# Optimization experiments

Hardware: AMD Instinct MI355X
Metric: run time of the kernel (lower is better)

## Reference

```python
import jax, jax.numpy as jnp
import numpy as np

B, L, D = 4, 8192, 512


def setup_inputs() -> dict:
    key = jax.random.key(0)
    kx, kwg, kwc = jax.random.split(key, 3)
    x = jax.random.normal(kx, (B, L, D), dtype=jnp.float32)
    # Xavier-uniform init for DxD linears
    bound = float(np.sqrt(6.0 / (D + D)))
    Wg = jax.random.uniform(kwg, (D, D), minval=-bound, maxval=bound, dtype=jnp.float32)
    bg = jnp.ones((D,), dtype=jnp.float32)   # gate bias init to 1.0
    Wc = jax.random.uniform(kwc, (D, D), minval=-bound, maxval=bound, dtype=jnp.float32)
    bc = jnp.zeros((D,), dtype=jnp.float32)
    return {"x": x, "Wg": Wg, "bg": bg, "Wc": Wc, "bc": bc}


def _mingru_scan(gates, cands):
    # h_t = (1 - g_t) * h_{t-1} + g_t * c_t, h_0 = 0
    # linear recurrence h_t = a_t h_{t-1} + b_t with a = 1-g, b = g*c
    a = 1.0 - gates
    b = gates * cands

    def combine(left, right):
        a_l, b_l = left
        a_r, b_r = right
        return a_r * a_l, a_r * b_l + b_r

    _, h = jax.lax.associative_scan(combine, (a, b), axis=1)
    return h


def reference(x, Wg, bg, Wc, bc):
    gates = jax.nn.sigmoid(jnp.einsum('bld,ed->ble', x, Wg) + bg)
    cands = jnp.tanh(jnp.einsum('bld,ed->ble', x, Wc) + bc)
    return _mingru_scan(gates, cands)
```

## Files before the change

### kernel.cpp

```cpp
#include <hip/hip_runtime.h>
#include <stdint.h>
#include <stddef.h>

#define B_ 4
#define L_ 8192
#define D_ 512
#define M_ (B_*L_)
#define K_ 512
#define CHUNK 64
#define NC (L_/CHUNK)

typedef _Float16 f16;
typedef f16 f16x2 __attribute__((ext_vector_type(2)));
typedef f16 f16x4 __attribute__((ext_vector_type(4)));
typedef f16 f16x8 __attribute__((ext_vector_type(8)));
typedef float f32x4 __attribute__((ext_vector_type(4)));

__device__ __forceinline__ void async16(const void* g, void* l) {
  __builtin_amdgcn_global_load_lds(
      (const __attribute__((address_space(1))) uint32_t*)g,
      (__attribute__((address_space(3))) uint32_t*)l,
      16, 0, 0);
}

__global__ __launch_bounds__(256) void prep(const float* __restrict__ x,
                                            const float* __restrict__ Wg,
                                            const float* __restrict__ Wc,
                                            f16* __restrict__ xh,
                                            f16* __restrict__ wp) {
  const int bid = blockIdx.x;
  const int isX = (bid < 8192);
  const int U = (isX ? bid : (bid - 8192)) * 256 + threadIdx.x;
  const int r  = U >> 6;
  const int w_ = U & 63;
  const int s  = w_ >> 3;
  const int u3 = w_ & 7;
  const int du = (r << 6) + (s << 3) + (u3 ^ (r & 7));
  const float* src;
  if (isX)            src = x + (size_t)U * 8;
  else if (r < 512)   src = Wg + (size_t)r * 512 + w_ * 8;
  else                src = Wc + (size_t)(r - 512) * 512 + w_ * 8;
  float4 v0 = *(const float4*)src;
  float4 v1 = *(const float4*)(src + 4);
  f16x8 o = {(f16)v0.x, (f16)v0.y, (f16)v0.z, (f16)v0.w,
             (f16)v1.x, (f16)v1.y, (f16)v1.z, (f16)v1.w};
  f16* dst = isX ? xh : wp;
  *(f16x8*)(dst + (size_t)du * 8) = o;
}

__global__ __launch_bounds__(512, 2) void gemm_act(
    const f16* __restrict__ Xh, const f16* __restrict__ Wp,
    const float* __restrict__ bg, const float* __restrict__ bc,
    uint32_t* __restrict__ AC,
    float* __restrict__ cA, float* __restrict__ cB) {
  __shared__ __align__(16) f16 sA[2][256 * 64];
  __shared__ __align__(16) f16 sBg[2][128 * 64];
  __shared__ __align__(16) f16 sBc[2][128 * 64];

  const int tid = threadIdx.x;
  const int id = blockIdx.x;
  const int xcd = id & 7;
  const int slot = id >> 3;
  const int g_ = xcd * 64 + slot;
  const int bm = g_ >> 2;
  const int bn = g_ & 3;

  const int lane = tid & 63;
  const int w = tid >> 6;
  const int wm = w >> 1, wn = w & 1;
  const int l15 = lane & 15, quad = lane >> 4;

  const int srow = tid >> 3;
  const int sp8 = (tid & 7) * 8;
  const f16* gA  = Xh + (size_t)(bm * 256 + srow) * K_ + sp8;
  const f16* gBg = Wp + (size_t)(bn * 128 + srow) * K_ + sp8;
  const f16* gBc = Wp + (size_t)(512 + bn * 128 + srow) * K_ + sp8;

  const int xu0 = (quad ^ (l15 & 7)) * 8;
  const int xu1 = xu0 ^ 32;

  f32x4 accG[4][4] = {};
  f32x4 accC[4][4] = {};

#define STAGE(kk, b) { \
    async16(gA + (kk),                    &sA[b][tid * 8]); \
    async16(gA + (size_t) 64 * K_ + (kk), &sA[b][tid * 8 +  64 * 64]); \
    async16(gA + (size_t)128 * K_ + (kk), &sA[b][tid * 8 + 128 * 64]); \
    async16(gA + (size_t)192 * K_ + (kk), &sA[b][tid * 8 + 192 * 64]); \
    async16(gBg + (kk),                   &sBg[b][tid * 8]); \
    async16(gBg + (size_t)64 * K_ + (kk), &sBg[b][tid * 8 + 64 * 64]); \
    async16(gBc + (kk),                   &sBc[b][tid * 8]); \
    async16(gBc + (size_t)64 * K_ + (kk), &sBc[b][tid * 8 + 64 * 64]); }

#define COMPUTE(bC) { \
    _Pragma("unroll") \
    for (int k32 = 0; k32 < 2; k32++) { \
      const int xu = k32 ? xu1 : xu0; \
      f16x8 af[4], bgf[4], bcf[4]; \
      _Pragma("unroll") \
      for (int i = 0; i < 4; i++) \
        af[i] = *(const f16x8*)(&sA[bC][(wm * 64 + i * 16 + l15) * 64 + xu]); \
      _Pragma("unroll") \
      for (int j = 0; j < 4; j++) { \
        bgf[j] = *(const f16x8*)(&sBg[bC][(wn * 64 + j * 16 + l15) * 64 + xu]); \
        bcf[j] = *(const f16x8*)(&sBc[bC][(wn * 64 + j * 16 + l15) * 64 + xu]); \
      } \
      _Pragma("unroll") \
      for (int i = 0; i < 4; i++) \
        _Pragma("unroll") \
        for (int j = 0; j < 4; j++) { \
          accG[i][j] = __builtin_amdgcn_mfma_f32_16x16x32_f16(af[i], bgf[j], accG[i][j], 0, 0, 0); \
          accC[i][j] = __builtin_amdgcn_mfma_f32_16x16x32_f16(af[i], bcf[j], accC[i][j], 0, 0, 0); \
        } \
    } }

  STAGE(0, 0);
  asm volatile("s_waitcnt vmcnt(0)" ::: "memory");
  __builtin_amdgcn_s_barrier();

#pragma unroll
  for (int t = 0; t < 7; t++) {
    const int c = t & 1, n = c ^ 1;
    STAGE((t + 1) * 64, n);
    COMPUTE(c);
    asm volatile("s_waitcnt vmcnt(0)" ::: "memory");
    __builtin_amdgcn_s_barrier();
  }
  COMPUTE(1);
#undef COMPUTE
#undef STAGE

  const int c = bm * 4 + wm;
#pragma unroll
  for (int j = 0; j < 4; j++) {
    const int col = bn * 128 + wn * 64 + j * 16 + l15;
    const float bgv = bg[col];
    const float bcv = bc[col];
    float blkP[4], blkQ[4];
#pragma unroll
    for (int i = 0; i < 4; i++) {
      const int mrow = bm * 256 + wm * 64 + i * 16 + quad * 4;
      float P = 1.0f, Q = 0.0f;
#pragma unroll
      for (int r = 0; r < 4; r++) {
        float yg = accG[i][j][r] + bgv;
        float gg = 1.0f / (1.0f + __expf(-yg));
        float yc = accC[i][j][r] + bcv;
        yc = fminf(fmaxf(yc, -15.0f), 15.0f);
        float t = __expf(2.0f * yc);
        float cc = (t - 1.0f) / (t + 1.0f);
        f16x2 p;
        p[0] = (f16)(1.0f - gg);
        p[1] = (f16)(gg * cc);
        *(f16x2*)&AC[(size_t)(mrow + r) * 512 + col] = p;
        const float av = (float)p[0];
        const float bv = (float)p[1];
        Q = fmaf(av, Q, bv);
        P *= av;
      }
      float Pp = __shfl_xor(P, 16);
      float Qp = __shfl_xor(Q, 16);
      float nP = P * Pp;
      float nQ = (quad & 1) ? fmaf(P, Qp, Q) : fmaf(Pp, Q, Qp);
      Pp = __shfl_xor(nP, 32);
      Qp = __shfl_xor(nQ, 32);
      blkP[i] = nP * Pp;
      blkQ[i] = (quad & 2) ? fmaf(nP, Qp, nQ) : fmaf(Pp, nQ, Qp);
    }
    float CP = blkP[0], CQ = blkQ[0];
#pragma unroll
    for (int i = 1; i < 4; i++) {
      CQ = fmaf(blkP[i], CQ, blkQ[i]);
      CP *= blkP[i];
    }
    if (quad == 0) {
      cA[(size_t)c * 512 + col] = CP;
      cB[(size_t)c * 512 + col] = CQ;
    }
  }
}

__global__ __launch_bounds__(128) void scan_apply(
    const uint32_t* __restrict__ AC,
    const float* __restrict__ cA, const float* __restrict__ cB,
    float* __restrict__ out) {
  const int blk = blockIdx.x;
  const int ch = blk & (NC - 1);
  const int bseq = blk >> 7;
  const int d0 = threadIdx.x * 4;

  float h0 = 0.0f, h1 = 0.0f, h2 = 0.0f, h3 = 0.0f;
  const float* pA = cA + (size_t)(bseq * NC) * 512 + d0;
  const float* pB = cB + (size_t)(bseq * NC) * 512 + d0;
#pragma unroll 4
  for (int cc = 0; cc < ch; cc++) {
    float4 va = *(const float4*)(pA + (size_t)cc * 512);
    float4 vb = *(const float4*)(pB + (size_t)cc * 512);
    h0 = fmaf(va.x, h0, vb.x);
    h1 = fmaf(va.y, h1, vb.y);
    h2 = fmaf(va.z, h2, vb.z);
    h3 = fmaf(va.w, h3, vb.w);
  }

  const size_t base = (size_t)blk * CHUNK * 512 + d0;
#pragma unroll 8
  for (int t = 0; t < CHUNK; t++) {
    const size_t i = base + (size_t)t * 512;
    uint4 v = *(const uint4*)&AC[i];
    f16x2 p0 = __builtin_bit_cast(f16x2, v.x);
    f16x2 p1 = __builtin_bit_cast(f16x2, v.y);
    f16x2 p2 = __builtin_bit_cast(f16x2, v.z);
    f16x2 p3 = __builtin_bit_cast(f16x2, v.w);
    h0 = fmaf((float)p0[0], h0, (float)p0[1]);
    h1 = fmaf((float)p1[0], h1, (float)p1[1]);
    h2 = fmaf((float)p2[0], h2, (float)p2[1]);
    h3 = fmaf((float)p3[0], h3, (float)p3[1]);
    float4 o;
    o.x = h0; o.y = h1; o.z = h2; o.w = h3;
    *(float4*)&out[i] = o;
  }
}

extern "C" void kernel_launch(void* const* d_in, const int* in_sizes, int n_in,
                              void* d_out, int out_size, void* d_ws, size_t ws_size,
                              hipStream_t stream) {
  const float* x  = (const float*)d_in[0];
  const float* Wg = (const float*)d_in[1];
  const float* bg = (const float*)d_in[2];
  const float* Wc = (const float*)d_in[3];
  const float* bc = (const float*)d_in[4];
  float* out = (float*)d_out;

  char* ws = (char*)d_ws;
  f16*      xh = (f16*)(ws);
  f16*      wp = (f16*)(ws + 33554432);
  uint32_t* AC = (uint32_t*)(ws + 34603008);
  float*    cA = (float*)(ws + 101711872);
  float*    cB = (float*)(ws + 102760448);

  prep<<<8448, 256, 0, stream>>>(x, Wg, Wc, xh, wp);
  gemm_act<<<512, 512, 0, stream>>>(xh, wp, bg, bc, AC, cA, cB);
  scan_apply<<<B_ * NC, 128, 0, stream>>>(AC, cA, cB, out);
}
```

Baseline: 228.3 us.

## Fuse GEMM, chunk scan and apply into one persistent kernel with grid barriers

```diff
diff --git a/kernel.cpp b/kernel.cpp
--- a/kernel.cpp
+++ b/kernel.cpp
@@ -12,7 +12,6 @@
 
 typedef _Float16 f16;
 typedef f16 f16x2 __attribute__((ext_vector_type(2)));
-typedef f16 f16x4 __attribute__((ext_vector_type(4)));
 typedef f16 f16x8 __attribute__((ext_vector_type(8)));
 typedef float f32x4 __attribute__((ext_vector_type(4)));
 
@@ -21,6 +20,13 @@
       (const __attribute__((address_space(1))) uint32_t*)g,
       (__attribute__((address_space(3))) uint32_t*)l,
       16, 0, 0);
+}
+
+__device__ __forceinline__ float aload(const float* p) {
+  return __hip_atomic_load(p, __ATOMIC_RELAXED, __HIP_MEMORY_SCOPE_AGENT);
+}
+__device__ __forceinline__ void astore(float* p, float v) {
+  __hip_atomic_store(p, v, __ATOMIC_RELAXED, __HIP_MEMORY_SCOPE_AGENT);
 }
 
 __global__ __launch_bounds__(256) void prep(const float* __restrict__ x,
@@ -48,176 +54,206 @@
   *(f16x8*)(dst + (size_t)du * 8) = o;
 }
 
-__global__ __launch_bounds__(512, 2) void gemm_act(
+__device__ __forceinline__ void gbar(int* cnt, int target) {
+  __threadfence();
+  __syncthreads();
+  if (threadIdx.x == 0) {
+    atomicAdd(cnt, 1);
+    while (__hip_atomic_load(cnt, __ATOMIC_RELAXED, __HIP_MEMORY_SCOPE_AGENT) < target)
+      __builtin_amdgcn_s_sleep(8);
+  }
+  __syncthreads();
+  __threadfence();
+}
+
+__global__ __launch_bounds__(512, 2) void fused(
     const f16* __restrict__ Xh, const f16* __restrict__ Wp,
     const float* __restrict__ bg, const float* __restrict__ bc,
-    uint32_t* __restrict__ AC,
-    float* __restrict__ cA, float* __restrict__ cB) {
-  __shared__ __align__(16) f16 sA[2][256 * 64];
+    float* __restrict__ cA, float* __restrict__ cB,
+    float* __restrict__ Hpre, int* __restrict__ bar,
+    float* __restrict__ out) {
+  __shared__ __align__(16) f16 sA[2][128 * 64];
   __shared__ __align__(16) f16 sBg[2][128 * 64];
   __shared__ __align__(16) f16 sBc[2][128 * 64];
 
   const int tid = threadIdx.x;
   const int id = blockIdx.x;
-  const int xcd = id & 7;
-  const int slot = id >> 3;
-  const int g_ = xcd * 64 + slot;
-  const int bm = g_ >> 2;
-  const int bn = g_ & 3;
+  const int bm = (id & 7) * 32 + (id >> 3);
 
   const int lane = tid & 63;
   const int w = tid >> 6;
-  const int wm = w >> 1, wn = w & 1;
+  const int wm = w >> 2, wn = w & 3;
   const int l15 = lane & 15, quad = lane >> 4;
 
   const int srow = tid >> 3;
   const int sp8 = (tid & 7) * 8;
-  const f16* gA  = Xh + (size_t)(bm * 256 + srow) * K_ + sp8;
-  const f16* gBg = Wp + (size_t)(bn * 128 + srow) * K_ + sp8;
-  const f16* gBc = Wp + (size_t)(512 + bn * 128 + srow) * K_ + sp8;
+  const f16* gA  = Xh + (size_t)(bm * 128 + srow) * K_ + sp8;
+  const f16* gBg = Wp + (size_t)srow * K_ + sp8;
+  const f16* gBc = Wp + (size_t)(512 + srow) * K_ + sp8;
 
   const int xu0 = (quad ^ (l15 & 7)) * 8;
   const int xu1 = xu0 ^ 32;
 
-  f32x4 accG[4][4] = {};
-  f32x4 accC[4][4] = {};
-
-#define STAGE(kk, b) { \
-    async16(gA + (kk),                    &sA[b][tid * 8]); \
-    async16(gA + (size_t) 64 * K_ + (kk), &sA[b][tid * 8 +  64 * 64]); \
-    async16(gA + (size_t)128 * K_ + (kk), &sA[b][tid * 8 + 128 * 64]); \
-    async16(gA + (size_t)192 * K_ + (kk), &sA[b][tid * 8 + 192 * 64]); \
-    async16(gBg + (kk),                   &sBg[b][tid * 8]); \
-    async16(gBg + (size_t)64 * K_ + (kk), &sBg[b][tid * 8 + 64 * 64]); \
-    async16(gBc + (kk),                   &sBc[b][tid * 8]); \
-    async16(gBc + (size_t)64 * K_ + (kk), &sBc[b][tid * 8 + 64 * 64]); }
+  const int c_ = bm * 2 + wm;
+  uint4 ab[4][4][2];
+
+#define STAGE(kk, b, bo) { \
+    async16(gA + (kk),                   &sA[b][tid * 8]); \
+    async16(gA + (size_t)64 * K_ + (kk), &sA[b][tid * 8 + 64 * 64]); \
+    async16(gBg + (bo) + (kk),                   &sBg[b][tid * 8]); \
+    async16(gBg + (bo) + (size_t)64 * K_ + (kk), &sBg[b][tid * 8 + 64 * 64]); \
+    async16(gBc + (bo) + (kk),                   &sBc[b][tid * 8]); \
+    async16(gBc + (bo) + (size_t)64 * K_ + (kk), &sBc[b][tid * 8 + 64 * 64]); }
 
 #define COMPUTE(bC) { \
     _Pragma("unroll") \
     for (int k32 = 0; k32 < 2; k32++) { \
       const int xu = k32 ? xu1 : xu0; \
-      f16x8 af[4], bgf[4], bcf[4]; \
+      f16x8 af[4], bgf[2], bcf[2]; \
       _Pragma("unroll") \
       for (int i = 0; i < 4; i++) \
         af[i] = *(const f16x8*)(&sA[bC][(wm * 64 + i * 16 + l15) * 64 + xu]); \
       _Pragma("unroll") \
-      for (int j = 0; j < 4; j++) { \
-        bgf[j] = *(const f16x8*)(&sBg[bC][(wn * 64 + j * 16 + l15) * 64 + xu]); \
-        bcf[j] = *(const f16x8*)(&sBc[bC][(wn * 64 + j * 16 + l15) * 64 + xu]); \
+      for (int j = 0; j < 2; j++) { \
+        bgf[j] = *(const f16x8*)(&sBg[bC][(wn * 32 + j * 16 + l15) * 64 + xu]); \
+        bcf[j] = *(const f16x8*)(&sBc[bC][(wn * 32 + j * 16 + l15) * 64 + xu]); \
       } \
       _Pragma("unroll") \
       for (int i = 0; i < 4; i++) \
         _Pragma("unroll") \
-        for (int j = 0; j < 4; j++) { \
+        for (int j = 0; j < 2; j++) { \
           accG[i][j] = __builtin_amdgcn_mfma_f32_16x16x32_f16(af[i], bgf[j], accG[i][j], 0, 0, 0); \
           accC[i][j] = __builtin_amdgcn_mfma_f32_16x16x32_f16(af[i], bcf[j], accC[i][j], 0, 0, 0); \
         } \
     } }
 
-  STAGE(0, 0);
-  asm volatile("s_waitcnt vmcnt(0)" ::: "memory");
-  __builtin_amdgcn_s_barrier();
-
-#pragma unroll
-  for (int t = 0; t < 7; t++) {
-    const int c = t & 1, n = c ^ 1;
-    STAGE((t + 1) * 64, n);
-    COMPUTE(c);
+#pragma unroll
+  for (int bn = 0; bn < 4; bn++) {
+    const size_t bo = (size_t)bn * 128 * K_;
+    f32x4 accG[4][2] = {};
+    f32x4 accC[4][2] = {};
+
+    STAGE(0, 0, bo);
     asm volatile("s_waitcnt vmcnt(0)" ::: "memory");
     __builtin_amdgcn_s_barrier();
-  }
-  COMPUTE(1);
+#pragma unroll
+    for (int t = 0; t < 7; t++) {
+      const int cb = t & 1, nb = cb ^ 1;
+      STAGE((t + 1) * 64, nb, bo);
+      COMPUTE(cb);
+      asm volatile("s_waitcnt vmcnt(0)" ::: "memory");
+      __builtin_amdgcn_s_barrier();
+    }
+    COMPUTE(1);
+
+#pragma unroll
+    for (int j = 0; j < 2; j++) {
+      const int col = bn * 128 + wn * 32 + j * 16 + l15;
+      const float bgv = bg[col];
+      const float bcv = bc[col];
+      float blkP[4], blkQ[4];
+#pragma unroll
+      for (int i = 0; i < 4; i++) {
+        float P = 1.0f, Q = 0.0f;
+        uint32_t pk[4];
+#pragma unroll
+        for (int r = 0; r < 4; r++) {
+          float yg = accG[i][j][r] + bgv;
+          float gg = 1.0f / (1.0f + __expf(-yg));
+          float yc = accC[i][j][r] + bcv;
+          yc = fminf(fmaxf(yc, -15.0f), 15.0f);
+          float tt = __expf(2.0f * yc);
+          float cc = (tt - 1.0f) / (tt + 1.0f);
+          f16x2 p;
+          p[0] = (f16)(1.0f - gg);
+          p[1] = (f16)(gg * cc);
+          pk[r] = __builtin_bit_cast(uint32_t, p);
+          const float av = (float)p[0];
+          const float bv = (float)p[1];
+          Q = fmaf(av, Q, bv);
+          P *= av;
+        }
+        ab[bn][i][j] = make_uint4(pk[0], pk[1], pk[2], pk[3]);
+        float Pp = __shfl_xor(P, 16);
+        float Qp = __shfl_xor(Q, 16);
+        float nP = P * Pp;
+        float nQ = (quad & 1) ? fmaf(P, Qp, Q) : fmaf(Pp, Q, Qp);
+        Pp = __shfl_xor(nP, 32);
+        Qp = __shfl_xor(nQ, 32);
+        blkP[i] = nP * Pp;
+        blkQ[i] = (quad & 2) ? fmaf(nP, Qp, nQ) : fmaf(Pp, nQ, Qp);
+      }
+      float CP = blkP[0], CQ = blkQ[0];
+#pragma unroll
+      for (int i = 1; i < 4; i++) {
+        CQ = fmaf(blkP[i], CQ, blkQ[i]);
+        CP *= blkP[i];
+      }
+      if (quad == 0) {
+        astore(&cA[(size_t)c_ * 512 + col], CP);
+        astore(&cB[(size_t)c_ * 512 + col], CQ);
+      }
+    }
+  }
 #undef COMPUTE
 #undef STAGE
 
-  const int c = bm * 4 + wm;
-#pragma unroll
-  for (int j = 0; j < 4; j++) {
-    const int col = bn * 128 + wn * 64 + j * 16 + l15;
-    const float bgv = bg[col];
-    const float bcv = bc[col];
-    float blkP[4], blkQ[4];
-#pragma unroll
-    for (int i = 0; i < 4; i++) {
-      const int mrow = bm * 256 + wm * 64 + i * 16 + quad * 4;
-      float P = 1.0f, Q = 0.0f;
-#pragma unroll
-      for (int r = 0; r < 4; r++) {
-        float yg = accG[i][j][r] + bgv;
-        float gg = 1.0f / (1.0f + __expf(-yg));
-        float yc = accC[i][j][r] + bcv;
-        yc = fminf(fmaxf(yc, -15.0f), 15.0f);
-        float t = __expf(2.0f * yc);
-        float cc = (t - 1.0f) / (t + 1.0f);
-        f16x2 p;
-        p[0] = (f16)(1.0f - gg);
-        p[1] = (f16)(gg * cc);
-        *(f16x2*)&AC[(size_t)(mrow + r) * 512 + col] = p;
-        const float av = (float)p[0];
-        const float bv = (float)p[1];
-        Q = fmaf(av, Q, bv);
-        P *= av;
-      }
-      float Pp = __shfl_xor(P, 16);
-      float Qp = __shfl_xor(Q, 16);
-      float nP = P * Pp;
-      float nQ = (quad & 1) ? fmaf(P, Qp, Q) : fmaf(Pp, Q, Qp);
-      Pp = __shfl_xor(nP, 32);
-      Qp = __shfl_xor(nQ, 32);
-      blkP[i] = nP * Pp;
-      blkQ[i] = (quad & 2) ? fmaf(nP, Qp, nQ) : fmaf(Pp, nQ, Qp);
-    }
-    float CP = blkP[0], CQ = blkQ[0];
-#pragma unroll
-    for (int i = 1; i < 4; i++) {
-      CQ = fmaf(blkP[i], CQ, blkQ[i]);
-      CP *= blkP[i];
-    }
-    if (quad == 0) {
-      cA[(size_t)c * 512 + col] = CP;
-      cB[(size_t)c * 512 + col] = CQ;
-    }
-  }
-}
-
-__global__ __launch_bounds__(128) void scan_apply(
-    const uint32_t* __restrict__ AC,
-    const float* __restrict__ cA, const float* __restrict__ cB,
-    float* __restrict__ out) {
-  const int blk = blockIdx.x;
-  const int ch = blk & (NC - 1);
-  const int bseq = blk >> 7;
-  const int d0 = threadIdx.x * 4;
-
-  float h0 = 0.0f, h1 = 0.0f, h2 = 0.0f, h3 = 0.0f;
-  const float* pA = cA + (size_t)(bseq * NC) * 512 + d0;
-  const float* pB = cB + (size_t)(bseq * NC) * 512 + d0;
-#pragma unroll 4
-  for (int cc = 0; cc < ch; cc++) {
-    float4 va = *(const float4*)(pA + (size_t)cc * 512);
-    float4 vb = *(const float4*)(pB + (size_t)cc * 512);
-    h0 = fmaf(va.x, h0, vb.x);
-    h1 = fmaf(va.y, h1, vb.y);
-    h2 = fmaf(va.z, h2, vb.z);
-    h3 = fmaf(va.w, h3, vb.w);
-  }
-
-  const size_t base = (size_t)blk * CHUNK * 512 + d0;
-#pragma unroll 8
-  for (int t = 0; t < CHUNK; t++) {
-    const size_t i = base + (size_t)t * 512;
-    uint4 v = *(const uint4*)&AC[i];
-    f16x2 p0 = __builtin_bit_cast(f16x2, v.x);
-    f16x2 p1 = __builtin_bit_cast(f16x2, v.y);
-    f16x2 p2 = __builtin_bit_cast(f16x2, v.z);
-    f16x2 p3 = __builtin_bit_cast(f16x2, v.w);
-    h0 = fmaf((float)p0[0], h0, (float)p0[1]);
-    h1 = fmaf((float)p1[0], h1, (float)p1[1]);
-    h2 = fmaf((float)p2[0], h2, (float)p2[1]);
-    h3 = fmaf((float)p3[0], h3, (float)p3[1]);
-    float4 o;
-    o.x = h0; o.y = h1; o.z = h2; o.w = h3;
-    *(float4*)&out[i] = o;
+  gbar(bar, 256);
+
+  if (id < 4) {
+    const int seq = blockIdx.x & 3;
+    const int d = tid;
+    float h = 0.0f;
+    for (int ch = 0; ch < NC; ch++) {
+      const int idx = (seq * NC + ch) * 512 + d;
+      astore(&Hpre[idx], h);
+      h = fmaf(aload(&cA[idx]), h, aload(&cB[idx]));
+    }
+  }
+
+  gbar(bar, 512);
+
+#pragma unroll
+  for (int bn = 0; bn < 4; bn++) {
+#pragma unroll
+    for (int j = 0; j < 2; j++) {
+      const int col = bn * 128 + wn * 32 + j * 16 + l15;
+      const float h0 = aload(&Hpre[(size_t)c_ * 512 + col]);
+      float iA = 1.0f, iB = 0.0f;
+#pragma unroll
+      for (int i = 0; i < 4; i++) {
+        const uint4 pk = ab[bn][i][j];
+        const f16x2 q0 = __builtin_bit_cast(f16x2, pk.x);
+        const f16x2 q1 = __builtin_bit_cast(f16x2, pk.y);
+        const f16x2 q2 = __builtin_bit_cast(f16x2, pk.z);
+        const f16x2 q3 = __builtin_bit_cast(f16x2, pk.w);
+        const float a0 = (float)q0[0], b0 = (float)q0[1];
+        const float a1 = (float)q1[0], b1 = (float)q1[1];
+        const float a2 = (float)q2[0], b2 = (float)q2[1];
+        const float a3 = (float)q3[0], b3 = (float)q3[1];
+        float P = a0, Q = b0;
+        Q = fmaf(a1, Q, b1); P *= a1;
+        Q = fmaf(a2, Q, b2); P *= a2;
+        Q = fmaf(a3, Q, b3); P *= a3;
+        float sP = P, sQ = Q;
+        float tP = __shfl_up(sP, 16), tQ = __shfl_up(sQ, 16);
+        if (quad >= 1) { sQ = fmaf(sP, tQ, sQ); sP *= tP; }
+        tP = __shfl_up(sP, 32); tQ = __shfl_up(sQ, 32);
+        if (quad >= 2) { sQ = fmaf(sP, tQ, sQ); sP *= tP; }
+        float xP = __shfl_up(sP, 16), xQ = __shfl_up(sQ, 16);
+        if (quad == 0) { xP = 1.0f; xQ = 0.0f; }
+        const float bPv = __shfl(sP, 48 + l15);
+        const float bQv = __shfl(sQ, 48 + l15);
+        float h = fmaf(xP, fmaf(iA, h0, iB), xQ);
+        const size_t rb = (size_t)(bm * 128 + wm * 64 + i * 16 + quad * 4) * 512 + col;
+        h = fmaf(a0, h, b0); out[rb]           = h;
+        h = fmaf(a1, h, b1); out[rb + 512]     = h;
+        h = fmaf(a2, h, b2); out[rb + 1024]    = h;
+        h = fmaf(a3, h, b3); out[rb + 1536]    = h;
+        iB = fmaf(bPv, iB, bQv);
+        iA *= bPv;
+      }
+    }
   }
 }
 
@@ -232,13 +268,14 @@
   float* out = (float*)d_out;
 
   char* ws = (char*)d_ws;
-  f16*      xh = (f16*)(ws);
-  f16*      wp = (f16*)(ws + 33554432);
-  uint32_t* AC = (uint32_t*)(ws + 34603008);
-  float*    cA = (float*)(ws + 101711872);
-  float*    cB = (float*)(ws + 102760448);
-
+  f16*   xh = (f16*)(ws);
+  f16*   wp = (f16*)(ws + 33554432);
+  float* cA = (float*)(ws + 34603008);
+  float* cB = (float*)(ws + 35651584);
+  float* Hp = (float*)(ws + 36700160);
+  int*   bar = (int*)(ws + 37748736);
+
+  hipMemsetAsync(bar, 0, sizeof(int), stream);
   prep<<<8448, 256, 0, stream>>>(x, Wg, Wc, xh, wp);
-  gemm_act<<<512, 512, 0, stream>>>(xh, wp, bg, bc, AC, cA, cB);
-  scan_apply<<<B_ * NC, 128, 0, stream>>>(AC, cA, cB, out);
-}
+  fused<<<256, 512, 0, stream>>>(xh, wp, bg, bc, cA, cB, Hp, bar, out);
+}
```

After: 403.1 us. 76.6% more time.
